# Performance work log

Hardware: AMD Instinct MI355X
Metric: run time of the kernel (lower is better)

Reference implementation:

```python
import jax, jax.numpy as jnp
import numpy as np

N_NODES = 100000
N_EDGES = 1600000
IN_F, HID, N_COLORS = 128, 128, 10


def setup_inputs() -> dict:
    key = jax.random.key(0)
    k1, k2, k3, k4 = jax.random.split(key, 4)
    x = jax.random.normal(k1, (N_NODES, IN_F), dtype=jnp.float32)
    edge_index = jax.random.randint(k2, (2, N_EDGES), 0, N_NODES, dtype=jnp.int64)
    # Glorot-ish init for weights
    W1 = jax.random.normal(k3, (IN_F, HID), dtype=jnp.float32) / np.sqrt(IN_F)
    b1 = jnp.zeros((HID,), dtype=jnp.float32)
    W2 = jax.random.normal(k4, (HID, N_COLORS), dtype=jnp.float32) / np.sqrt(HID)
    b2 = jnp.zeros((N_COLORS,), dtype=jnp.float32)
    return {"x": x, "edge_index": edge_index, "W1": W1, "b1": b1, "W2": W2, "b2": b2}


def _gcn_norm(edge_index, num_nodes):
    # Add self-loops, compute symmetric normalization D^-1/2 (A+I) D^-1/2
    loops = jnp.arange(num_nodes, dtype=edge_index.dtype)
    src = jnp.concatenate([edge_index[0], loops])
    dst = jnp.concatenate([edge_index[1], loops])
    deg = jax.ops.segment_sum(jnp.ones_like(dst, dtype=jnp.float32), dst,
                              num_segments=num_nodes)
    deg_isqrt = jax.lax.rsqrt(deg)  # deg >= 1 due to self-loops
    norm = deg_isqrt[src] * deg_isqrt[dst]  # [E + N]
    return src, dst, norm


def _gcn_conv(h, src, dst, norm, num_nodes, W, b):
    # Linear transform first (PyG GCNConv), then gather-scale-scatter aggregate
    h = h @ W                                   # [N, out]
    msg = h[src] * norm[:, None]                # [E + N, out] gather
    out = jax.ops.segment_sum(msg, dst, num_segments=num_nodes)  # scatter-add
    return out + b


def reference(x, edge_index, W1, b1, W2, b2):
    n = x.shape[0]
    src, dst, norm = _gcn_norm(edge_index, n)
    h = _gcn_conv(x, src, dst, norm, n, W1, b1)
    h = jax.nn.relu(h)
    # dropout is identity in eval mode
    h = _gcn_conv(h, src, dst, norm, n, W2, b2)
    return jax.nn.softmax(h, axis=1)
```

## Files before the change

### kernel.cpp

```cpp
#include <hip/hip_runtime.h>
#include <hip/hip_fp16.h>

#define IN_F 128
#define HID  128
#define NC   10
#define H2P  16
#define NPB  128
#define NBMAX 784
#define BCAP 2560
#define CAPP 2944
#define EPB  4096
#define LDW  136

typedef _Float16 f16x8 __attribute__((ext_vector_type(8)));
typedef float f32x4 __attribute__((ext_vector_type(4)));
typedef int int4a __attribute__((ext_vector_type(4), aligned(4)));

__device__ inline __half2 shfl_xor_h2(__half2 v, int mask) {
    int i = __shfl_xor(*reinterpret_cast<int*>(&v), mask, 64);
    return *reinterpret_cast<__half2*>(&i);
}

__global__ __launch_bounds__(1024) void k_bin(const int* __restrict__ src,
                                              const int* __restrict__ dst,
                                              int* __restrict__ bcnt,
                                              unsigned int* __restrict__ binned,
                                              const float* __restrict__ W1,
                                              __half* __restrict__ WT,
                                              const float* __restrict__ W2,
                                              float* __restrict__ W2T,
                                              int E, int nbin) {
    __shared__ int hist[NBMAX];
    __shared__ int base[NBMAX];
    __shared__ int lcur[NBMAX];
    const int tid = threadIdx.x;

    if (blockIdx.x == 0) {
        for (int i = tid; i < IN_F * HID; i += 1024) {
            int k = i >> 7, n = i & 127;
            WT[n * IN_F + k] = __float2half(W1[k * HID + n]);
        }
        for (int i = tid; i < NC * IN_F; i += 1024)
            W2T[i] = W2[(i & 127) * NC + (i >> 7)];
    }

    for (int b = tid; b < nbin; b += 1024) { hist[b] = 0; lcur[b] = 0; }
    __syncthreads();

    const int e0 = blockIdx.x * EPB + tid;
    int d[4];
    #pragma unroll
    for (int u = 0; u < 4; u++) {
        int e = e0 + u * 1024;
        d[u] = (e < E) ? dst[e] : -1;
        if (d[u] >= 0) atomicAdd(&hist[d[u] >> 7], 1);
    }
    __syncthreads();
    for (int b = tid; b < nbin; b += 1024) {
        int h = hist[b];
        base[b] = h ? atomicAdd(&bcnt[b], h) : 0;
    }
    __syncthreads();
    #pragma unroll
    for (int u = 0; u < 4; u++) {
        int e = e0 + u * 1024;
        if (e < E) {
            int dd = d[u];
            int b = dd >> 7;
            int s = src[e];
            int o = base[b] + atomicAdd(&lcur[b], 1);
            if (o < BCAP)
                binned[(size_t)b * BCAP + o] = ((unsigned)(dd & 127) << 17) | (unsigned)s;
        }
    }
}

__global__ __launch_bounds__(512) void k_pg(const int* __restrict__ bcnt,
                                            const unsigned int* __restrict__ binned,
                                            int2* __restrict__ rowinfo,
                                            float* __restrict__ dis,
                                            int* __restrict__ csr,
                                            const float* __restrict__ X,
                                            const __half* __restrict__ WT,
                                            __half* __restrict__ hsh,
                                            __half* __restrict__ h2h,
                                            int N) {
    __shared__ int h[NPB];
    __shared__ int lb[NPB];
    __shared__ int cur[NPB];
    __shared__ float sdis[NPB];
    __shared__ _Float16 sX[2][32 * LDW];
    __shared__ _Float16 sW[128 * LDW];
    const int b = blockIdx.x;
    const int tid = threadIdx.x;

    if (tid < NPB) h[tid] = 0;
    __syncthreads();

    const int m = min(bcnt[b], BCAP);
    const unsigned int* p = binned + (size_t)b * BCAP;
    for (int i = tid; i < m; i += 512) atomicAdd(&h[p[i] >> 17], 1);
    __syncthreads();

    int myh = 0, cnt4 = 0;
    if (tid < NPB) { myh = h[tid]; cnt4 = (myh + 3) & ~3; lb[tid] = cnt4; }
    __syncthreads();
    #pragma unroll
    for (int off = 1; off < NPB; off <<= 1) {
        int t = (tid < NPB && tid >= off) ? lb[tid - off] : 0;
        __syncthreads();
        if (tid < NPB) lb[tid] += t;
        __syncthreads();
    }
    int ex = 0;
    if (tid < NPB) {
        ex = lb[tid] - cnt4;
        int node = b * NPB + tid;
        if (node < N) {
            rowinfo[node] = make_int2(b * CAPP + ex, cnt4);
            float dd = rsqrtf(1.0f + (float)myh);
            dis[node] = dd;
            sdis[tid] = dd;
        }
        lb[tid] = ex;
        cur[tid] = 0;
    }
    __syncthreads();
    for (int i = tid; i < m; i += 512) {
        unsigned v = p[i];
        int dl = v >> 17;
        int r = atomicAdd(&cur[dl], 1);
        csr[b * CAPP + lb[dl] + r] = (int)(v & 0x1FFFF);
    }
    if (tid < NPB) {
        for (int k = myh; k < cnt4; k++) csr[b * CAPP + ex + k] = N;
    }
    if (b == 0) {
        f16x8 z = {0, 0, 0, 0, 0, 0, 0, 0};
        if (tid < 16) *(f16x8*)(hsh + (size_t)N * HID + tid * 8) = z;
        if (tid < 2)  *(f16x8*)(h2h + (size_t)N * H2P + tid * 8) = z;
    }

    {
        int n = tid >> 2, part = tid & 3;
        const f16x8* srcp = (const f16x8*)(WT + n * IN_F);
        f16x8* dstp = (f16x8*)(sW + n * LDW);
        #pragma unroll
        for (int c = 0; c < 4; c++) dstp[part * 4 + c] = srcp[part * 4 + c];
    }

    const int wave = tid >> 6;
    const int grp  = wave >> 2;
    const int nbase = (wave & 3) * 32;
    const int lane = tid & 63;
    const int quad = lane >> 4;
    const int l16 = lane & 15;
    const int sub256 = tid >> 8;
    const int t256 = tid & 255;

    for (int t = 0; t < 2; t++) {
        __syncthreads();
        {
            int tdx = 2 * t + sub256;
            int r = t256 >> 3;
            int k0 = (t256 & 7) * 16;
            int row = b * NPB + tdx * 32 + r;
            if (row >= N) row = N - 1;
            const float* sp = X + (size_t)row * IN_F + k0;
            float4 f0 = *(const float4*)(sp);
            float4 f1 = *(const float4*)(sp + 4);
            float4 f2 = *(const float4*)(sp + 8);
            float4 f3 = *(const float4*)(sp + 12);
            f16x8 h0, h1;
            h0[0] = (_Float16)f0.x; h0[1] = (_Float16)f0.y;
            h0[2] = (_Float16)f0.z; h0[3] = (_Float16)f0.w;
            h0[4] = (_Float16)f1.x; h0[5] = (_Float16)f1.y;
            h0[6] = (_Float16)f1.z; h0[7] = (_Float16)f1.w;
            h1[0] = (_Float16)f2.x; h1[1] = (_Float16)f2.y;
            h1[2] = (_Float16)f2.z; h1[3] = (_Float16)f2.w;
            h1[4] = (_Float16)f3.x; h1[5] = (_Float16)f3.y;
            h1[6] = (_Float16)f3.z; h1[7] = (_Float16)f3.w;
            *(f16x8*)(sX[sub256] + r * LDW + k0) = h0;
            *(f16x8*)(sX[sub256] + r * LDW + k0 + 8) = h1;
        }
        __syncthreads();

        const int tdx = 2 * t + grp;
        f32x4 acc00 = {0,0,0,0}, acc01 = {0,0,0,0}, acc10 = {0,0,0,0}, acc11 = {0,0,0,0};
        #pragma unroll
        for (int kc = 0; kc < 4; kc++) {
            const int koff = kc * 32 + quad * 8;
            f16x8 a0 = *(const f16x8*)(sX[grp] + l16 * LDW + koff);
            f16x8 a1 = *(const f16x8*)(sX[grp] + (16 + l16) * LDW + koff);
            f16x8 b0 = *(const f16x8*)(sW + (nbase + l16) * LDW + koff);
            f16x8 b1 = *(const f16x8*)(sW + (nbase + 16 + l16) * LDW + koff);
            acc00 = __builtin_amdgcn_mfma_f32_16x16x32_f16(a0, b0, acc00, 0, 0, 0);
            acc01 = __builtin_amdgcn_mfma_f32_16x16x32_f16(a0, b1, acc01, 0, 0, 0);
            acc10 = __builtin_amdgcn_mfma_f32_16x16x32_f16(a1, b0, acc10, 0, 0, 0);
            acc11 = __builtin_amdgcn_mfma_f32_16x16x32_f16(a1, b1, acc11, 0, 0, 0);
        }
        #pragma unroll
        for (int r = 0; r < 4; r++) {
            {
                int lr = tdx * 32 + quad * 4 + r;
                int row = b * NPB + lr;
                if (row < N) {
                    float d = sdis[lr];
                    __half* o = hsh + (size_t)row * HID + nbase + l16;
                    o[0]  = __float2half(acc00[r] * d);
                    o[16] = __float2half(acc01[r] * d);
                }
            }
            {
                int lr = tdx * 32 + 16 + quad * 4 + r;
                int row = b * NPB + lr;
                if (row < N) {
                    float d = sdis[lr];
                    __half* o = hsh + (size_t)row * HID + nbase + l16;
                    o[0]  = __float2half(acc10[r] * d);
                    o[16] = __float2half(acc11[r] * d);
                }
            }
        }
    }
}

__global__ __launch_bounds__(256) void k_agg1(const __half* __restrict__ hsh,
                                              const int2* __restrict__ rowinfo,
                                              const int* __restrict__ csr,
                                              const float* __restrict__ dis,
                                              const float* __restrict__ b1,
                                              const float* __restrict__ W2T,
                                              __half* __restrict__ h2h,
                                              int base0, int nend) {
    const int node = base0 + blockIdx.x * 4 + (threadIdx.x >> 6);
    if (node >= nend) return;
    const int lane = threadIdx.x & 63;
    const int g   = lane >> 4;
    const int l16 = lane & 15;
    const int f0  = l16 * 8;
    const __half2 hz = __half2half2(__float2half(0.0f));

    const int2 ri = rowinfo[node];
    const int beg = ri.x, end = ri.x + ri.y;
    const float d = dis[node];

    __half2 acc2[4] = {hz, hz, hz, hz};
    if (g == 0) {
        float4 r = *(const float4*)(hsh + (size_t)node * HID + f0);
        const __half2* hh = (const __half2*)&r;
        acc2[0] = hh[0]; acc2[1] = hh[1]; acc2[2] = hh[2]; acc2[3] = hh[3];
    }

    int j0 = beg + 4 * g;
    if (j0 < end) {
        int4a cv0 = *(const int4a*)(csr + j0);
        int  j1 = j0 + 16;
        bool m1 = j1 < end;
        int4a cv1 = m1 ? *(const int4a*)(csr + j1) : cv0;
        float4 r0 = *(const float4*)(hsh + (size_t)cv0[0] * HID + f0);
        float4 r1 = *(const float4*)(hsh + (size_t)cv0[1] * HID + f0);
        float4 r2 = *(const float4*)(hsh + (size_t)cv0[2] * HID + f0);
        float4 r3 = *(const float4*)(hsh + (size_t)cv0[3] * HID + f0);
        while (true) {
            const int  j2 = j1 + 16;
            const bool m2 = m1 && (j2 < end);
            int4a cv2 = m2 ? *(const int4a*)(csr + j2) : cv1;
            float4 n0, n1, n2, n3;
            if (m1) {
                n0 = *(const float4*)(hsh + (size_t)cv1[0] * HID + f0);
                n1 = *(const float4*)(hsh + (size_t)cv1[1] * HID + f0);
                n2 = *(const float4*)(hsh + (size_t)cv1[2] * HID + f0);
                n3 = *(const float4*)(hsh + (size_t)cv1[3] * HID + f0);
            }
            const __half2* h0 = (const __half2*)&r0;
            const __half2* h1 = (const __half2*)&r1;
            const __half2* h2 = (const __half2*)&r2;
            const __half2* h3 = (const __half2*)&r3;
            #pragma unroll
            for (int i = 0; i < 4; i++) {
                acc2[i] = __hadd2(acc2[i], h0[i]);
                acc2[i] = __hadd2(acc2[i], h1[i]);
                acc2[i] = __hadd2(acc2[i], h2[i]);
                acc2[i] = __hadd2(acc2[i], h3[i]);
            }
            if (!m1) break;
            r0 = n0; r1 = n1; r2 = n2; r3 = n3;
            cv1 = cv2; m1 = m2; j1 = j2;
        }
    }

    #pragma unroll
    for (int i = 0; i < 4; i++) {
        acc2[i] = __hadd2(acc2[i], shfl_xor_h2(acc2[i], 16));
        acc2[i] = __hadd2(acc2[i], shfl_xor_h2(acc2[i], 32));
    }
    float acc[8];
    #pragma unroll
    for (int i = 0; i < 4; i++) {
        float2 t = __half22float2(acc2[i]);
        acc[2 * i] = t.x; acc[2 * i + 1] = t.y;
    }

    float4 ba = *(const float4*)(b1 + f0);
    float4 bb = *(const float4*)(b1 + f0 + 4);
    float h[8];
    h[0] = fmaxf(fmaf(d, acc[0], ba.x), 0.0f);
    h[1] = fmaxf(fmaf(d, acc[1], ba.y), 0.0f);
    h[2] = fmaxf(fmaf(d, acc[2], ba.z), 0.0f);
    h[3] = fmaxf(fmaf(d, acc[3], ba.w), 0.0f);
    h[4] = fmaxf(fmaf(d, acc[4], bb.x), 0.0f);
    h[5] = fmaxf(fmaf(d, acc[5], bb.y), 0.0f);
    h[6] = fmaxf(fmaf(d, acc[6], bb.z), 0.0f);
    h[7] = fmaxf(fmaf(d, acc[7], bb.w), 0.0f);

    const int cb = (g == 0) ? 0 : (g == 1) ? 3 : (g == 2) ? 6 : 8;
    const int nc = (g < 2) ? 3 : 2;
    float p[3];
    #pragma unroll
    for (int ci = 0; ci < 3; ci++) {
        if (ci < nc) {
            int c = cb + ci;
            float4 wa = *(const float4*)(W2T + c * IN_F + f0);
            float4 wb = *(const float4*)(W2T + c * IN_F + f0 + 4);
            float t = fmaf(h[0], wa.x, fmaf(h[1], wa.y, fmaf(h[2], wa.z, h[3] * wa.w)));
            t = fmaf(h[4], wb.x, fmaf(h[5], wb.y, fmaf(h[6], wb.z, fmaf(h[7], wb.w, t))));
            #pragma unroll
            for (int off = 1; off < 16; off <<= 1) t += __shfl_xor(t, off, 64);
            p[ci] = t;
        }
    }
    if (l16 == 0) {
        __half* o = h2h + (size_t)node * H2P + cb;
        for (int ci = 0; ci < nc; ci++) o[ci] = __float2half(d * p[ci]);
    }
}

__global__ __launch_bounds__(256) void k_agg2(const __half* __restrict__ h2h,
                                              const int2* __restrict__ rowinfo,
                                              const int* __restrict__ csr,
                                              const float* __restrict__ dis,
                                              const float* __restrict__ b2,
                                              float* __restrict__ out,
                                              int N) {
    int t = blockIdx.x * 256 + threadIdx.x;
    int node = t >> 3;
    if (node >= N) return;
    int o = t & 7;
    int q = o & 1;
    int eg = o >> 1;
    const int base = q * 8;
    const __half2 hz = __half2half2(__float2half(0.0f));

    __half2 a2[4] = {hz, hz, hz, hz};
    if (eg == 0) {
        float4 r = *(const float4*)(h2h + (size_t)node * H2P + base);
        const __half2* hh = (const __half2*)&r;
        a2[0] = hh[0]; a2[1] = hh[1]; a2[2] = hh[2]; a2[3] = hh[3];
    }
    const int2 ri = rowinfo[node];
    const int end = ri.x + ri.y;

    int j0 = ri.x + 4 * eg;
    if (j0 < end) {
        int4a cv0 = *(const int4a*)(csr + j0);
        int  j1 = j0 + 16;
        bool m1 = j1 < end;
        int4a cv1 = m1 ? *(const int4a*)(csr + j1) : cv0;
        float4 r0 = *(const float4*)(h2h + (size_t)cv0[0] * H2P + base);
        float4 r1 = *(const float4*)(h2h + (size_t)cv0[1] * H2P + base);
        float4 r2 = *(const float4*)(h2h + (size_t)cv0[2] * H2P + base);
        float4 r3 = *(const float4*)(h2h + (size_t)cv0[3] * H2P + base);
        while (true) {
            const int  j2 = j1 + 16;
            const bool m2 = m1 && (j2 < end);
            int4a cv2 = m2 ? *(const int4a*)(csr + j2) : cv1;
            float4 n0, n1, n2, n3;
            if (m1) {
                n0 = *(const float4*)(h2h + (size_t)cv1[0] * H2P + base);
                n1 = *(const float4*)(h2h + (size_t)cv1[1] * H2P + base);
                n2 = *(const float4*)(h2h + (size_t)cv1[2] * H2P + base);
                n3 = *(const float4*)(h2h + (size_t)cv1[3] * H2P + base);
            }
            const __half2* h0 = (const __half2*)&r0;
            const __half2* h1 = (const __half2*)&r1;
            const __half2* h2 = (const __half2*)&r2;
            const __half2* h3 = (const __half2*)&r3;
            #pragma unroll
            for (int i = 0; i < 4; i++) {
                a2[i] = __hadd2(a2[i], h0[i]);
                a2[i] = __hadd2(a2[i], h1[i]);
                a2[i] = __hadd2(a2[i], h2[i]);
                a2[i] = __hadd2(a2[i], h3[i]);
            }
            if (!m1) break;
            r0 = n0; r1 = n1; r2 = n2; r3 = n3;
            cv1 = cv2; m1 = m2; j1 = j2;
        }
    }

    #pragma unroll
    for (int i = 0; i < 4; i++) {
        a2[i] = __hadd2(a2[i], shfl_xor_h2(a2[i], 2));
        a2[i] = __hadd2(a2[i], shfl_xor_h2(a2[i], 4));
    }

    float a[8];
    #pragma unroll
    for (int i = 0; i < 4; i++) {
        float2 tt = __half22float2(a2[i]);
        a[2 * i] = tt.x; a[2 * i + 1] = tt.y;
    }

    const float d = dis[node];
    float vv[8];
    #pragma unroll
    for (int i = 0; i < 8; i++) {
        int f = base + i;
        vv[i] = (f < NC) ? fmaf(d, a[i], b2[f]) : -1e30f;
    }
    float m = vv[0];
    #pragma unroll
    for (int i = 1; i < 8; i++) m = fmaxf(m, vv[i]);
    m = fmaxf(m, __shfl_xor(m, 1, 64));
    float e[8];
    float s = 0.0f;
    #pragma unroll
    for (int i = 0; i < 8; i++) { e[i] = (base + i < NC) ? expf(vv[i] - m) : 0.0f; s += e[i]; }
    s += __shfl_xor(s, 1, 64);
    float inv = 1.0f / s;

    float* op = out + (size_t)node * NC;
    if (o == 0) {
        *(float2*)(op + 0) = make_float2(e[0] * inv, e[1] * inv);
        *(float2*)(op + 2) = make_float2(e[2] * inv, e[3] * inv);
        *(float2*)(op + 4) = make_float2(e[4] * inv, e[5] * inv);
        *(float2*)(op + 6) = make_float2(e[6] * inv, e[7] * inv);
    } else if (o == 1) {
        *(float2*)(op + 8) = make_float2(e[0] * inv, e[1] * inv);
    }
}

extern "C" void kernel_launch(void* const* d_in, const int* in_sizes, int n_in,
                              void* d_out, int out_size, void* d_ws, size_t ws_size,
                              hipStream_t stream) {
    const float* x  = (const float*)d_in[0];
    const int*   ei = (const int*)d_in[1];
    const float* W1 = (const float*)d_in[2];
    const float* b1 = (const float*)d_in[3];
    const float* W2 = (const float*)d_in[4];
    const float* b2 = (const float*)d_in[5];
    float* out = (float*)d_out;

    const int N = in_sizes[0] / IN_F;
    const int E = in_sizes[1] / 2;
    const int* esrc = ei;
    const int* edst = ei + E;
    const int nbin = (N + NPB - 1) / NPB;

    char* ws = (char*)d_ws;
    int2*   rowinfo = (int2*)(ws);
    float*  dis     = (float*)(ws + 0x100000);
    int*    bcnt    = (int*)(ws + 0x180000);
    __half* WT      = (__half*)(ws + 0x190000);
    float*  W2T     = (float*)(ws + 0x1A0000);
    unsigned int* binned = (unsigned int*)(ws + 0x200000);
    int*    csr     = (int*)(ws + 0xA00000);
    __half* hsh     = (__half*)(ws + 0x1400000);
    __half* h2h     = (__half*)(ws + 0x2D00000);

    hipMemsetAsync(bcnt, 0, (size_t)nbin * sizeof(int), stream);

    k_bin <<<(E + EPB - 1) / EPB, 1024, 0, stream>>>(esrc, edst, bcnt, binned, W1, WT, W2, W2T, E, nbin);
    k_pg  <<<nbin, 512, 0, stream>>>(bcnt, binned, rowinfo, dis, csr, x, WT, hsh, h2h, N);
    const int half = ((N / 2) + 3) & ~3;
    k_agg1<<<(half + 3) / 4, 256, 0, stream>>>(hsh, rowinfo, csr, dis, b1, W2T, h2h, 0, half);
    k_agg1<<<((N - half) + 3) / 4, 256, 0, stream>>>(hsh, rowinfo, csr, dis, b1, W2T, h2h, half, N);
    k_agg2<<<(int)(((size_t)N * 8 + 255) / 256), 256, 0, stream>>>(h2h, rowinfo, csr, dis, b2, out, N);
}
```

Measured before the change: 232.2 us.

## Stage binned edges in shared memory for coalesced writes; wave-shuffle scan; merge agg1 launches

The binning kernel now sorts each block's edges by bin in shared memory, using a block-wide prefix scan, before writing them out. Each bin's entries then go to global memory as contiguous runs instead of scattered single-word stores. The per-bin scan in k_pg switches from a shared-memory loop with many barriers to wavefront shuffles plus a two-wave combine. The two half-size k_agg1 launches become one launch. The cost is extra shared memory and a 1024-wide scan with many barriers in k_bin, which may reduce occupancy.

```diff
diff --git a/kernel.cpp b/kernel.cpp
--- a/kernel.cpp
+++ b/kernel.cpp
@@ -32,7 +32,11 @@
                                               int E, int nbin) {
     __shared__ int hist[NBMAX];
     __shared__ int base[NBMAX];
+    __shared__ int lofs[NBMAX];
     __shared__ int lcur[NBMAX];
+    __shared__ int scan[1024];
+    __shared__ unsigned int stage[EPB];
+    __shared__ unsigned short sbin[EPB];
     const int tid = threadIdx.x;
 
     if (blockIdx.x == 0) {
@@ -48,11 +52,12 @@
     __syncthreads();
 
     const int e0 = blockIdx.x * EPB + tid;
-    int d[4];
+    int d[4], s[4];
     #pragma unroll
     for (int u = 0; u < 4; u++) {
         int e = e0 + u * 1024;
         d[u] = (e < E) ? dst[e] : -1;
+        s[u] = (e < E) ? src[e] : 0;
         if (d[u] >= 0) atomicAdd(&hist[d[u] >> 7], 1);
     }
     __syncthreads();
@@ -60,18 +65,31 @@
         int h = hist[b];
         base[b] = h ? atomicAdd(&bcnt[b], h) : 0;
     }
+    scan[tid] = (tid < nbin) ? hist[tid] : 0;
+    __syncthreads();
+    for (int off = 1; off < 1024; off <<= 1) {
+        int t = (tid >= off) ? scan[tid - off] : 0;
+        __syncthreads();
+        scan[tid] += t;
+        __syncthreads();
+    }
+    if (tid < nbin) lofs[tid] = scan[tid] - hist[tid];
     __syncthreads();
     #pragma unroll
     for (int u = 0; u < 4; u++) {
-        int e = e0 + u * 1024;
-        if (e < E) {
-            int dd = d[u];
-            int b = dd >> 7;
-            int s = src[e];
-            int o = base[b] + atomicAdd(&lcur[b], 1);
-            if (o < BCAP)
-                binned[(size_t)b * BCAP + o] = ((unsigned)(dd & 127) << 17) | (unsigned)s;
-        }
+        if (d[u] >= 0) {
+            int b = d[u] >> 7;
+            int slot = lofs[b] + atomicAdd(&lcur[b], 1);
+            stage[slot] = ((unsigned)(d[u] & 127) << 17) | (unsigned)s[u];
+            sbin[slot] = (unsigned short)b;
+        }
+    }
+    __syncthreads();
+    const int total = scan[1023];
+    for (int i = tid; i < total; i += 1024) {
+        int b = sbin[i];
+        int o = base[b] + (i - lofs[b]);
+        if (o < BCAP) binned[(size_t)b * BCAP + o] = stage[i];
     }
 }
 
@@ -89,6 +107,7 @@
     __shared__ int lb[NPB];
     __shared__ int cur[NPB];
     __shared__ float sdis[NPB];
+    __shared__ int wtot[2];
     __shared__ _Float16 sX[2][32 * LDW];
     __shared__ _Float16 sW[128 * LDW];
     const int b = blockIdx.x;
@@ -103,18 +122,20 @@
     __syncthreads();
 
     int myh = 0, cnt4 = 0;
-    if (tid < NPB) { myh = h[tid]; cnt4 = (myh + 3) & ~3; lb[tid] = cnt4; }
-    __syncthreads();
-    #pragma unroll
-    for (int off = 1; off < NPB; off <<= 1) {
-        int t = (tid < NPB && tid >= off) ? lb[tid - off] : 0;
-        __syncthreads();
-        if (tid < NPB) lb[tid] += t;
-        __syncthreads();
-    }
+    if (tid < NPB) { myh = h[tid]; cnt4 = (myh + 3) & ~3; }
+    int inc = cnt4;
+    if (tid < NPB) {
+        #pragma unroll
+        for (int off = 1; off < 64; off <<= 1) {
+            int t = __shfl_up(inc, off, 64);
+            if ((tid & 63) >= off) inc += t;
+        }
+        if ((tid & 63) == 63) wtot[tid >> 6] = inc;
+    }
+    __syncthreads();
     int ex = 0;
     if (tid < NPB) {
-        ex = lb[tid] - cnt4;
+        ex = inc - cnt4 + ((tid >= 64) ? wtot[0] : 0);
         int node = b * NPB + tid;
         if (node < N) {
             rowinfo[node] = make_int2(b * CAPP + ex, cnt4);
@@ -232,9 +253,9 @@
                                               const float* __restrict__ b1,
                                               const float* __restrict__ W2T,
                                               __half* __restrict__ h2h,
-                                              int base0, int nend) {
-    const int node = base0 + blockIdx.x * 4 + (threadIdx.x >> 6);
-    if (node >= nend) return;
+                                              int N) {
+    const int node = blockIdx.x * 4 + (threadIdx.x >> 6);
+    if (node >= N) return;
     const int lane = threadIdx.x & 63;
     const int g   = lane >> 4;
     const int l16 = lane & 15;
@@ -473,8 +494,6 @@
 
     k_bin <<<(E + EPB - 1) / EPB, 1024, 0, stream>>>(esrc, edst, bcnt, binned, W1, WT, W2, W2T, E, nbin);
     k_pg  <<<nbin, 512, 0, stream>>>(bcnt, binned, rowinfo, dis, csr, x, WT, hsh, h2h, N);
-    const int half = ((N / 2) + 3) & ~3;
-    k_agg1<<<(half + 3) / 4, 256, 0, stream>>>(hsh, rowinfo, csr, dis, b1, W2T, h2h, 0, half);
-    k_agg1<<<((N - half) + 3) / 4, 256, 0, stream>>>(hsh, rowinfo, csr, dis, b1, W2T, h2h, half, N);
+    k_agg1<<<(N + 3) / 4, 256, 0, stream>>>(hsh, rowinfo, csr, dis, b1, W2T, h2h, N);
     k_agg2<<<(int)(((size_t)N * 8 + 255) / 256), 256, 0, stream>>>(h2h, rowinfo, csr, dis, b2, out, N);
 }
```

Result: faster. 224.5 us (-3.3%).
